# Kernel tuning notes

Measured on AMD Instinct MI355X. Metric: run time of the kernel, lower is better.

The kernel has to match this reference:

```python
import jax, jax.numpy as jnp
import numpy as np

N, F, H, C, HX, E = 50000, 256, 128, 16, 64, 500000
TEMP = 1.0


def gcn_conv(x, src, dst, W, b, n):
    # PyG GCNConv: x @ W, add self-loops, sym-normalized scatter-sum src->dst
    xw = x @ W
    idx = jnp.arange(n)
    s = jnp.concatenate([src, idx])
    d = jnp.concatenate([dst, idx])
    deg = jax.ops.segment_sum(jnp.ones_like(s, dtype=xw.dtype), d, num_segments=n)
    dinv = jnp.where(deg > 0, jax.lax.rsqrt(deg), 0.0)
    norm = dinv[s] * dinv[d]
    out = jax.ops.segment_sum(xw[s] * norm[:, None], d, num_segments=n)
    return out + b


def setup_inputs() -> dict:
    key = jax.random.key(0)
    ks = jax.random.split(key, 16)
    x = jax.random.normal(ks[0], (N, F), jnp.float32)
    edge_index = jax.random.randint(ks[1], (2, E), 0, N)
    neg_edge_index = jax.random.randint(ks[2], (2, E), 0, N)
    y = jax.random.randint(ks[3], (N,), 0, C)
    train_mask = jax.random.uniform(ks[4], (N,)) < 0.5
    def lin(k, fi, fo):
        s = 1.0 / np.sqrt(fi)
        return jax.random.uniform(k, (fi, fo), jnp.float32, -s, s)
    W1 = lin(ks[5], F, H); b1 = jnp.zeros((H,), jnp.float32)
    W2 = lin(ks[6], H, C); b2 = jnp.zeros((C,), jnp.float32)
    Wx = lin(ks[7], F, HX); bx = jnp.zeros((HX,), jnp.float32)
    Wd = lin(ks[8], 2 * (HX + C), 1); bd = jnp.zeros((1,), jnp.float32)
    return dict(x=x, edge_index=edge_index, neg_edge_index=neg_edge_index, y=y,
                train_mask=train_mask, W1=W1, b1=b1, W2=W2, b2=b2,
                Wx=Wx, bx=bx, Wd=Wd, bd=bd)


def reference(x, edge_index, neg_edge_index, y, train_mask,
              W1, b1, W2, b2, Wx, bx, Wd, bd):
    n = x.shape[0]
    # GNN encoder p(y|x,G): 2-layer GCN (eval mode -> dropout identity)
    h = jax.nn.relu(gcn_conv(x, edge_index[0], edge_index[1], W1, b1, n))
    logits = gcn_conv(h, edge_index[0], edge_index[1], W2, b2, n) / TEMP
    y_log_prob = jax.nn.log_softmax(logits, axis=-1)
    y_prob = jnp.where(train_mask[:, None],
                       jax.nn.one_hot(y, logits.shape[-1], dtype=logits.dtype),
                       jnp.exp(y_log_prob))
    # node feature encoder
    xe = jax.nn.relu(x @ Wx + bx)
    def decode(ei):
        s, d = ei[0], ei[1]
        feat = jnp.concatenate([xe[s], xe[d], y_prob[s], y_prob[d]], axis=1)
        return feat @ Wd + bd
    e_pred_pos = decode(edge_index)
    e_pred_neg = decode(neg_edge_index)
    return e_pred_pos, e_pred_neg, y_log_prob
```

## Files before the change

kernel.cpp:

```cpp
#include <hip/hip_runtime.h>

typedef unsigned short ushort_t;
typedef __attribute__((ext_vector_type(8))) short short8;
typedef __attribute__((ext_vector_type(4))) float floatx4;

constexpr int F = 256, H = 128, C = 16, HX = 64;
constexpr int NBCOL = H + HX;

__device__ __forceinline__ ushort_t f2bf(float f) {
  unsigned u = __float_as_uint(f);
  u += 0x7fffu + ((u >> 16) & 1u);
  return (ushort_t)(u >> 16);
}
__device__ __forceinline__ float bflo(unsigned u) { return __uint_as_float(u << 16); }
__device__ __forceinline__ float bfhi(unsigned u) { return __uint_as_float(u & 0xffff0000u); }

__global__ void k_pre(const float* __restrict__ x, ushort_t* __restrict__ xb, int total8,
                      const float* __restrict__ W1, const float* __restrict__ Wx,
                      ushort_t* __restrict__ WBt,
                      const int* __restrict__ dst, int* __restrict__ deg, int e,
                      int nbx, int nbw) {
  int b = blockIdx.x;
  if (b < nbx) {
    int i = b * 256 + threadIdx.x;
    if (i >= total8) return;
    const float4* xp = (const float4*)x;
    float4 a = xp[2 * i], bb = xp[2 * i + 1];
    ushort4 lo = make_ushort4(f2bf(a.x), f2bf(a.y), f2bf(a.z), f2bf(a.w));
    ushort4 hi = make_ushort4(f2bf(bb.x), f2bf(bb.y), f2bf(bb.z), f2bf(bb.w));
    ((ushort4*)xb)[2 * i] = lo;
    ((ushort4*)xb)[2 * i + 1] = hi;
  } else if (b < nbx + nbw) {
    int i = (b - nbx) * 256 + threadIdx.x;
    if (i >= NBCOL * F) return;
    int nn = i / F, k = i % F;
    float v = (nn < H) ? W1[k * H + nn] : Wx[k * HX + (nn - H)];
    WBt[nn * F + k] = f2bf(v);
  } else {
    int i = (b - nbx - nbw) * 256 + threadIdx.x;
    if (i < e) atomicAdd(&deg[dst[i]], 1);
  }
}

__global__ void k_scan_a(const int* __restrict__ deg, int* __restrict__ part, int n) {
  __shared__ int sm[256];
  int i = blockIdx.x * 256 + threadIdx.x;
  int v = (i < n) ? deg[i] : 0;
  sm[threadIdx.x] = v;
  __syncthreads();
  for (int s = 128; s > 0; s >>= 1) {
    if (threadIdx.x < s) sm[threadIdx.x] += sm[threadIdx.x + s];
    __syncthreads();
  }
  if (threadIdx.x == 0) part[blockIdx.x] = sm[0];
}

__global__ void k_scan_b(const int* __restrict__ part, int* __restrict__ blockoff, int nparts) {
  __shared__ int sm[256];
  int t = threadIdx.x;
  int v = (t < nparts) ? part[t] : 0;
  sm[t] = v;
  __syncthreads();
  for (int d = 1; d < 256; d <<= 1) {
    int add = (t >= d) ? sm[t - d] : 0;
    __syncthreads();
    sm[t] += add;
    __syncthreads();
  }
  blockoff[t] = sm[t] - v;
}

__global__ void k_scan_c(const int* __restrict__ deg, const int* __restrict__ blockoff,
                         int* __restrict__ row_start, int* __restrict__ cursor,
                         float* __restrict__ dinv, int n, int e) {
  int i = blockIdx.x * 256 + threadIdx.x;
  int lane = threadIdx.x & 63, wid = threadIdx.x >> 6;
  int v = (i < n) ? deg[i] : 0;
  int x = v;
  for (int d = 1; d < 64; d <<= 1) {
    int t = __shfl_up(x, d);
    if (lane >= d) x += t;
  }
  __shared__ int wsum[4], woff[4];
  if (lane == 63) wsum[wid] = x;
  __syncthreads();
  if (threadIdx.x == 0) {
    int s = 0;
    for (int w = 0; w < 4; w++) { woff[w] = s; s += wsum[w]; }
  }
  __syncthreads();
  int excl = x - v + woff[wid] + blockoff[blockIdx.x];
  if (i < n) {
    row_start[i] = excl;
    cursor[i] = excl;
    dinv[i] = rsqrtf((float)(v + 1));
  }
  if (i == 0) row_start[n] = e;
}

__global__ void k_fill(const int* __restrict__ src, const int* __restrict__ dst,
                       const float* __restrict__ dinv, int* __restrict__ cursor,
                       int2* __restrict__ csr8, int e) {
  int i = blockIdx.x * 256 + threadIdx.x;
  if (i < e) {
    int s = src[i];
    int p = atomicAdd(&cursor[dst[i]], 1);
    csr8[p] = make_int2(s, __float_as_int(dinv[s]));
  }
}

__global__ __launch_bounds__(256, 3) void k_gemm1(const ushort_t* __restrict__ xb,
                                                  const ushort_t* __restrict__ WBt,
                                                  const float* __restrict__ bx,
                                                  ushort_t* __restrict__ xw1,
                                                  float* __restrict__ xe,
                                                  int n, int ntiles) {
  int w = threadIdx.x >> 6, lane = threadIdx.x & 63;
  int q = lane >> 4, l15 = lane & 15;
  const short8* bb = (const short8*)WBt;
  short8 bfr[3][8];
#pragma unroll
  for (int t = 0; t < 3; t++)
#pragma unroll
    for (int kk = 0; kk < 8; kk++)
      bfr[t][kk] = bb[(size_t)(w * 48 + t * 16 + l15) * 32 + kk * 4 + q];

  float bxv[3];
#pragma unroll
  for (int t = 0; t < 3; t++) {
    int g = w * 48 + t * 16;
    bxv[t] = (g >= H) ? bx[g - H + l15] : 0.0f;
  }

  for (int tile = blockIdx.x; tile < ntiles; tile += gridDim.x) {
    int row = tile * 16 + l15;
    const short8* arow = (const short8*)(xb + (size_t)min(row, n - 1) * F);
    short8 a[8];
#pragma unroll
    for (int kk = 0; kk < 8; kk++) a[kk] = arow[kk * 4 + q];

    floatx4 acc0 = (floatx4)(0.0f), acc1 = (floatx4)(0.0f), acc2 = (floatx4)(0.0f);
#pragma unroll
    for (int kk = 0; kk < 8; kk++) {
      acc0 = __builtin_amdgcn_mfma_f32_16x16x32_bf16(a[kk], bfr[0][kk], acc0, 0, 0, 0);
      acc1 = __builtin_amdgcn_mfma_f32_16x16x32_bf16(a[kk], bfr[1][kk], acc1, 0, 0, 0);
      acc2 = __builtin_amdgcn_mfma_f32_16x16x32_bf16(a[kk], bfr[2][kk], acc2, 0, 0, 0);
    }

    floatx4 accs[3] = {acc0, acc1, acc2};
    int rbase = tile * 16 + q * 4;
#pragma unroll
    for (int t = 0; t < 3; t++) {
      int g = w * 48 + t * 16;
#pragma unroll
      for (int r = 0; r < 4; r++) {
        int ro = rbase + r;
        if (ro < n) {
          if (g < H) {
            xw1[(size_t)ro * H + g + l15] = f2bf(accs[t][r]);
          } else {
            xe[(size_t)ro * HX + (g - H) + l15] = fmaxf(accs[t][r] + bxv[t], 0.0f);
          }
        }
      }
    }
  }
}

__global__ void k_agg1(const ushort_t* __restrict__ xw1, const int* __restrict__ row_start,
                       const int2* __restrict__ csr8, const float* __restrict__ dinv,
                       const float* __restrict__ b1, ushort_t* __restrict__ hb, int n) {
  int v = blockIdx.x * 4 + (threadIdx.x >> 6);
  if (v >= n) return;
  int lane = threadIdx.x & 63;
  float dv = dinv[v];
  unsigned sv = ((const unsigned*)(xw1 + (size_t)v * H))[lane];
  float ax = dv * bflo(sv), ay = dv * bfhi(sv);
  int j0 = row_start[v], j1 = row_start[v + 1];
  int j = j0;
  for (; j + 8 <= j1; j += 8) {
    int2 ee[8];
    unsigned rr[8];
#pragma unroll
    for (int u = 0; u < 8; u++) ee[u] = csr8[j + u];
#pragma unroll
    for (int u = 0; u < 8; u++)
      rr[u] = ((const unsigned*)(xw1 + (size_t)ee[u].x * H))[lane];
#pragma unroll
    for (int u = 0; u < 8; u++) {
      float wu = __int_as_float(ee[u].y);
      ax += wu * bflo(rr[u]);
      ay += wu * bfhi(rr[u]);
    }
  }
  for (; j < j1; j++) {
    int2 e0 = csr8[j];
    unsigned r0 = ((const unsigned*)(xw1 + (size_t)e0.x * H))[lane];
    float w0 = __int_as_float(e0.y);
    ax += w0 * bflo(r0);
    ay += w0 * bfhi(r0);
  }
  int c = lane * 2;
  float o0 = fmaxf(dv * ax + b1[c], 0.0f);
  float o1 = fmaxf(dv * ay + b1[c + 1], 0.0f);
  unsigned hv = (unsigned)f2bf(o0) | ((unsigned)f2bf(o1) << 16);
  ((unsigned*)(hb + (size_t)v * H))[lane] = hv;
}

__global__ void k_gemm2(const ushort_t* __restrict__ hb, const float* __restrict__ W2,
                        float* __restrict__ hw2, int n) {
  int idx = blockIdx.x * 256 + threadIdx.x;
  int node = idx >> 2, cg = idx & 3;
  if (node >= n) return;
  float a0 = 0, a1 = 0, a2 = 0, a3 = 0;
  const unsigned* hr = (const unsigned*)(hb + (size_t)node * H);
#pragma unroll 8
  for (int k2 = 0; k2 < 64; k2++) {
    unsigned u = hr[k2];
    float h0 = bflo(u), h1 = bfhi(u);
    float4 w0 = *(const float4*)(W2 + (2 * k2) * C + cg * 4);
    float4 w1 = *(const float4*)(W2 + (2 * k2 + 1) * C + cg * 4);
    a0 += h0 * w0.x + h1 * w1.x;
    a1 += h0 * w0.y + h1 * w1.y;
    a2 += h0 * w0.z + h1 * w1.z;
    a3 += h0 * w0.w + h1 * w1.w;
  }
  *(float4*)(hw2 + (size_t)node * C + cg * 4) = make_float4(a0, a1, a2, a3);
}

__global__ void k_agg2ab(const float* __restrict__ hw2, const int* __restrict__ row_start,
                         const int2* __restrict__ csr8, const float* __restrict__ dinv,
                         const float* __restrict__ b2, const int* __restrict__ y,
                         const int* __restrict__ tmask, const float* __restrict__ xe,
                         const float* __restrict__ Wd, float* __restrict__ ylp_out,
                         float* __restrict__ Aarr, float* __restrict__ Barr, int n) {
  int idx = blockIdx.x * 256 + threadIdx.x;
  int node = idx >> 4, c = idx & 15;
  if (node >= n) return;
  float dv = dinv[node];
  float acc = dv * hw2[(size_t)node * C + c];
  int j0 = row_start[node], j1 = row_start[node + 1];
  int j = j0;
  for (; j + 8 <= j1; j += 8) {
    int2 ee[8];
    float rr[8];
#pragma unroll
    for (int u = 0; u < 8; u++) ee[u] = csr8[j + u];
#pragma unroll
    for (int u = 0; u < 8; u++) rr[u] = hw2[(size_t)ee[u].x * C + c];
#pragma unroll
    for (int u = 0; u < 8; u++) acc += __int_as_float(ee[u].y) * rr[u];
  }
  for (; j + 4 <= j1; j += 4) {
    int2 e0 = csr8[j], e1 = csr8[j + 1], e2 = csr8[j + 2], e3 = csr8[j + 3];
    float r0 = hw2[(size_t)e0.x * C + c];
    float r1 = hw2[(size_t)e1.x * C + c];
    float r2 = hw2[(size_t)e2.x * C + c];
    float r3 = hw2[(size_t)e3.x * C + c];
    acc += __int_as_float(e0.y) * r0 + __int_as_float(e1.y) * r1 +
           __int_as_float(e2.y) * r2 + __int_as_float(e3.y) * r3;
  }
  for (; j < j1; j++) {
    int2 e0 = csr8[j];
    acc += __int_as_float(e0.y) * hw2[(size_t)e0.x * C + c];
  }
  float logit = dv * acc + b2[c];
  float m = logit;
  for (int o = 8; o > 0; o >>= 1) m = fmaxf(m, __shfl_xor(m, o, 16));
  float e = expf(logit - m);
  float s16 = e;
  for (int o = 8; o > 0; o >>= 1) s16 += __shfl_xor(s16, o, 16);
  float lp = (logit - m) - logf(s16);
  ylp_out[(size_t)node * C + c] = lp;
  float yp = tmask[node] ? ((y[node] == c) ? 1.0f : 0.0f) : (e / s16);

  float4 xv = *(const float4*)(xe + (size_t)node * HX + c * 4);
  float4 wa = *(const float4*)(Wd + c * 4);
  float4 wb = *(const float4*)(Wd + HX + c * 4);
  float pa = xv.x * wa.x + xv.y * wa.y + xv.z * wa.z + xv.w * wa.w + yp * Wd[2 * HX + c];
  float pb = xv.x * wb.x + xv.y * wb.y + xv.z * wb.z + xv.w * wb.w + yp * Wd[2 * HX + C + c];
  for (int o = 8; o > 0; o >>= 1) {
    pa += __shfl_xor(pa, o, 16);
    pb += __shfl_xor(pb, o, 16);
  }
  if (c == 0) { Aarr[node] = pa; Barr[node] = pb; }
}

__global__ void k_decode(const int* __restrict__ ei, const int* __restrict__ nei,
                         const float* __restrict__ Aarr, const float* __restrict__ Barr,
                         const float* __restrict__ bd, float* __restrict__ out, int e) {
  int i = blockIdx.x * 256 + threadIdx.x;
  if (i >= 2 * e) return;
  float b0 = bd[0];
  if (i < e) {
    int s = ei[i], d = ei[e + i];
    out[i] = Aarr[s] + Barr[d] + b0;
  } else {
    int j = i - e;
    int s = nei[j], d = nei[e + j];
    out[e + j] = Aarr[s] + Barr[d] + b0;
  }
}

extern "C" void kernel_launch(void* const* d_in, const int* in_sizes, int n_in,
                              void* d_out, int out_size, void* d_ws, size_t ws_size,
                              hipStream_t stream) {
  const float* x = (const float*)d_in[0];
  const int* ei = (const int*)d_in[1];
  const int* nei = (const int*)d_in[2];
  const int* y = (const int*)d_in[3];
  const int* tmask = (const int*)d_in[4];
  const float* W1 = (const float*)d_in[5];
  const float* b1 = (const float*)d_in[6];
  const float* W2 = (const float*)d_in[7];
  const float* b2 = (const float*)d_in[8];
  const float* Wx = (const float*)d_in[9];
  const float* bx = (const float*)d_in[10];
  const float* Wd = (const float*)d_in[11];
  const float* bd = (const float*)d_in[12];
  float* out = (float*)d_out;

  int n = in_sizes[3];
  int e = in_sizes[1] / 2;

  char* ws = (char*)d_ws;
  size_t off = 0;
  auto alloc = [&](size_t bytes) -> void* {
    void* p = ws + off;
    off += (bytes + 511) & ~(size_t)511;
    return p;
  };
  ushort_t* xb = (ushort_t*)alloc((size_t)n * F * 2);
  ushort_t* WBt = (ushort_t*)alloc((size_t)NBCOL * F * 2);
  ushort_t* xw1 = (ushort_t*)alloc((size_t)n * H * 2);
  float* xe = (float*)alloc((size_t)n * HX * 4);
  ushort_t* hb = (ushort_t*)alloc((size_t)n * H * 2);
  float* hw2 = (float*)alloc((size_t)n * C * 4);
  float* dinv = (float*)alloc((size_t)n * 4);
  int* deg = (int*)alloc((size_t)n * 4);
  int* row_start = (int*)alloc((size_t)(n + 1) * 4);
  int* cursor = (int*)alloc((size_t)n * 4);
  int2* csr8 = (int2*)alloc((size_t)e * 8);
  int* part = (int*)alloc(1024 * 4);
  int* blockoff = (int*)alloc(1024 * 4);
  float* Aarr = (float*)alloc((size_t)n * 4);
  float* Barr = (float*)alloc((size_t)n * 4);

  const int* src = ei;
  const int* dst = ei + e;

  hipMemsetAsync(deg, 0, (size_t)n * 4, stream);

  int total8 = n * F / 8;
  int nbx = (total8 + 255) / 256;
  int nbw = (NBCOL * F + 255) / 256;
  int nbe = (e + 255) / 256;
  k_pre<<<nbx + nbw + nbe, 256, 0, stream>>>(x, xb, total8, W1, Wx, WBt, dst, deg, e,
                                             nbx, nbw);

  int nblk = (n + 255) / 256;
  k_scan_a<<<nblk, 256, 0, stream>>>(deg, part, n);
  k_scan_b<<<1, 256, 0, stream>>>(part, blockoff, nblk);
  k_scan_c<<<nblk, 256, 0, stream>>>(deg, blockoff, row_start, cursor, dinv, n, e);
  k_fill<<<(e + 255) / 256, 256, 0, stream>>>(src, dst, dinv, cursor, csr8, e);

  int ntiles = (n + 15) / 16;
  int ggrid = ntiles < 768 ? ntiles : 768;
  k_gemm1<<<ggrid, 256, 0, stream>>>(xb, WBt, bx, xw1, xe, n, ntiles);
  k_agg1<<<(n + 3) / 4, 256, 0, stream>>>(xw1, row_start, csr8, dinv, b1, hb, n);
  k_gemm2<<<(n * 4 + 255) / 256, 256, 0, stream>>>(hb, W2, hw2, n);
  k_agg2ab<<<(n * 16 + 255) / 256, 256, 0, stream>>>(hw2, row_start, csr8, dinv, b2, y,
                                                     tmask, xe, Wd, out + (size_t)2 * e,
                                                     Aarr, Barr, n);
  k_decode<<<(2 * e + 255) / 256, 256, 0, stream>>>(ei, nei, Aarr, Barr, bd, out, e);
}
```

Baseline: 269.8 us.

## Fuse preprocessing, CSR build and GEMM1 into persistent kernel; fuse agg1 with GEMM2

Merges the conversion, degree counting, three scan kernels, CSR fill and the first GEMM into one persistent 512-block kernel. The stages are separated by atomic-counter grid barriers. The first aggregation now does the H×C projection through shared memory, so the bf16 hidden buffer and the separate GEMM2 launch are gone. The goal is to cut launch overhead and one intermediate global round trip. In exchange it relies on all 512 blocks being co-resident for the spin barriers, and the GEMM phase runs at fewer blocks and lower occupancy than before.

```diff
diff --git a/kernel.cpp b/kernel.cpp
--- a/kernel.cpp
+++ b/kernel.cpp
@@ -15,107 +15,111 @@
 __device__ __forceinline__ float bflo(unsigned u) { return __uint_as_float(u << 16); }
 __device__ __forceinline__ float bfhi(unsigned u) { return __uint_as_float(u & 0xffff0000u); }
 
-__global__ void k_pre(const float* __restrict__ x, ushort_t* __restrict__ xb, int total8,
-                      const float* __restrict__ W1, const float* __restrict__ Wx,
-                      ushort_t* __restrict__ WBt,
-                      const int* __restrict__ dst, int* __restrict__ deg, int e,
-                      int nbx, int nbw) {
-  int b = blockIdx.x;
-  if (b < nbx) {
-    int i = b * 256 + threadIdx.x;
-    if (i >= total8) return;
-    const float4* xp = (const float4*)x;
+__device__ __forceinline__ void gbar(int* cnt) {
+  __threadfence();
+  __syncthreads();
+  if (threadIdx.x == 0) {
+    __hip_atomic_fetch_add(cnt, 1, __ATOMIC_ACQ_REL, __HIP_MEMORY_SCOPE_AGENT);
+    while (__hip_atomic_load(cnt, __ATOMIC_ACQUIRE, __HIP_MEMORY_SCOPE_AGENT) <
+           (int)gridDim.x)
+      __builtin_amdgcn_s_sleep(2);
+  }
+  __syncthreads();
+}
+
+__global__ __launch_bounds__(256, 2) void k_build(
+    const float* __restrict__ x, ushort_t* __restrict__ xb, int total8,
+    const float* __restrict__ W1, const float* __restrict__ Wx,
+    ushort_t* __restrict__ WBt, const int* __restrict__ src,
+    const int* __restrict__ dst, int* __restrict__ deg, int e,
+    int* __restrict__ part, int* __restrict__ blockoff,
+    int* __restrict__ row_start, int* __restrict__ cursor,
+    float* __restrict__ dinv, int2* __restrict__ csr8,
+    const float* __restrict__ bx, ushort_t* __restrict__ xw1,
+    float* __restrict__ xe, int* __restrict__ bar, int n, int ntiles) {
+  __shared__ int sm[256];
+  __shared__ int wsum[4], woff[4];
+  int tid = blockIdx.x * 256 + threadIdx.x;
+  int nthreads = gridDim.x * 256;
+  int lane = threadIdx.x & 63, wid = threadIdx.x >> 6;
+
+  const float4* xp = (const float4*)x;
+  for (int i = tid; i < total8; i += nthreads) {
     float4 a = xp[2 * i], bb = xp[2 * i + 1];
     ushort4 lo = make_ushort4(f2bf(a.x), f2bf(a.y), f2bf(a.z), f2bf(a.w));
     ushort4 hi = make_ushort4(f2bf(bb.x), f2bf(bb.y), f2bf(bb.z), f2bf(bb.w));
     ((ushort4*)xb)[2 * i] = lo;
     ((ushort4*)xb)[2 * i + 1] = hi;
-  } else if (b < nbx + nbw) {
-    int i = (b - nbx) * 256 + threadIdx.x;
-    if (i >= NBCOL * F) return;
+  }
+  for (int i = tid; i < NBCOL * F; i += nthreads) {
     int nn = i / F, k = i % F;
     float v = (nn < H) ? W1[k * H + nn] : Wx[k * HX + (nn - H)];
     WBt[nn * F + k] = f2bf(v);
-  } else {
-    int i = (b - nbx - nbw) * 256 + threadIdx.x;
-    if (i < e) atomicAdd(&deg[dst[i]], 1);
-  }
-}
-
-__global__ void k_scan_a(const int* __restrict__ deg, int* __restrict__ part, int n) {
-  __shared__ int sm[256];
-  int i = blockIdx.x * 256 + threadIdx.x;
-  int v = (i < n) ? deg[i] : 0;
-  sm[threadIdx.x] = v;
-  __syncthreads();
-  for (int s = 128; s > 0; s >>= 1) {
-    if (threadIdx.x < s) sm[threadIdx.x] += sm[threadIdx.x + s];
-    __syncthreads();
-  }
-  if (threadIdx.x == 0) part[blockIdx.x] = sm[0];
-}
-
-__global__ void k_scan_b(const int* __restrict__ part, int* __restrict__ blockoff, int nparts) {
-  __shared__ int sm[256];
-  int t = threadIdx.x;
-  int v = (t < nparts) ? part[t] : 0;
-  sm[t] = v;
-  __syncthreads();
-  for (int d = 1; d < 256; d <<= 1) {
-    int add = (t >= d) ? sm[t - d] : 0;
-    __syncthreads();
-    sm[t] += add;
-    __syncthreads();
-  }
-  blockoff[t] = sm[t] - v;
-}
-
-__global__ void k_scan_c(const int* __restrict__ deg, const int* __restrict__ blockoff,
-                         int* __restrict__ row_start, int* __restrict__ cursor,
-                         float* __restrict__ dinv, int n, int e) {
-  int i = blockIdx.x * 256 + threadIdx.x;
-  int lane = threadIdx.x & 63, wid = threadIdx.x >> 6;
-  int v = (i < n) ? deg[i] : 0;
-  int x = v;
-  for (int d = 1; d < 64; d <<= 1) {
-    int t = __shfl_up(x, d);
-    if (lane >= d) x += t;
-  }
-  __shared__ int wsum[4], woff[4];
-  if (lane == 63) wsum[wid] = x;
-  __syncthreads();
-  if (threadIdx.x == 0) {
-    int s = 0;
-    for (int w = 0; w < 4; w++) { woff[w] = s; s += wsum[w]; }
-  }
-  __syncthreads();
-  int excl = x - v + woff[wid] + blockoff[blockIdx.x];
-  if (i < n) {
-    row_start[i] = excl;
-    cursor[i] = excl;
-    dinv[i] = rsqrtf((float)(v + 1));
-  }
-  if (i == 0) row_start[n] = e;
-}
-
-__global__ void k_fill(const int* __restrict__ src, const int* __restrict__ dst,
-                       const float* __restrict__ dinv, int* __restrict__ cursor,
-                       int2* __restrict__ csr8, int e) {
-  int i = blockIdx.x * 256 + threadIdx.x;
-  if (i < e) {
+  }
+  for (int i = tid; i < e; i += nthreads) atomicAdd(&deg[dst[i]], 1);
+  gbar(&bar[0]);
+
+  int nchunk = (n + 255) / 256;
+  for (int c = blockIdx.x; c < nchunk; c += gridDim.x) {
+    int i = c * 256 + threadIdx.x;
+    sm[threadIdx.x] = (i < n) ? deg[i] : 0;
+    __syncthreads();
+    for (int s = 128; s > 0; s >>= 1) {
+      if (threadIdx.x < s) sm[threadIdx.x] += sm[threadIdx.x + s];
+      __syncthreads();
+    }
+    if (threadIdx.x == 0) part[c] = sm[0];
+    __syncthreads();
+  }
+  gbar(&bar[1]);
+
+  if (blockIdx.x == 0) {
+    int t = threadIdx.x;
+    int v = (t < nchunk) ? part[t] : 0;
+    sm[t] = v;
+    __syncthreads();
+    for (int d = 1; d < 256; d <<= 1) {
+      int add = (t >= d) ? sm[t - d] : 0;
+      __syncthreads();
+      sm[t] += add;
+      __syncthreads();
+    }
+    blockoff[t] = sm[t] - v;
+  }
+  gbar(&bar[2]);
+
+  for (int c = blockIdx.x; c < nchunk; c += gridDim.x) {
+    int i = c * 256 + threadIdx.x;
+    int v = (i < n) ? deg[i] : 0;
+    int xs = v;
+    for (int d = 1; d < 64; d <<= 1) {
+      int t = __shfl_up(xs, d);
+      if (lane >= d) xs += t;
+    }
+    if (lane == 63) wsum[wid] = xs;
+    __syncthreads();
+    if (threadIdx.x == 0) {
+      int s = 0;
+      for (int w = 0; w < 4; w++) { woff[w] = s; s += wsum[w]; }
+    }
+    __syncthreads();
+    int excl = xs - v + woff[wid] + blockoff[c];
+    if (i < n) {
+      row_start[i] = excl;
+      cursor[i] = excl;
+      dinv[i] = rsqrtf((float)(v + 1));
+    }
+    __syncthreads();
+  }
+  if (tid == 0) row_start[n] = e;
+  gbar(&bar[3]);
+
+  for (int i = tid; i < e; i += nthreads) {
     int s = src[i];
     int p = atomicAdd(&cursor[dst[i]], 1);
     csr8[p] = make_int2(s, __float_as_int(dinv[s]));
   }
-}
-
-__global__ __launch_bounds__(256, 3) void k_gemm1(const ushort_t* __restrict__ xb,
-                                                  const ushort_t* __restrict__ WBt,
-                                                  const float* __restrict__ bx,
-                                                  ushort_t* __restrict__ xw1,
-                                                  float* __restrict__ xe,
-                                                  int n, int ntiles) {
-  int w = threadIdx.x >> 6, lane = threadIdx.x & 63;
+
   int q = lane >> 4, l15 = lane & 15;
   const short8* bb = (const short8*)WBt;
   short8 bfr[3][8];
@@ -123,22 +127,19 @@
   for (int t = 0; t < 3; t++)
 #pragma unroll
     for (int kk = 0; kk < 8; kk++)
-      bfr[t][kk] = bb[(size_t)(w * 48 + t * 16 + l15) * 32 + kk * 4 + q];
-
+      bfr[t][kk] = bb[(size_t)(wid * 48 + t * 16 + l15) * 32 + kk * 4 + q];
   float bxv[3];
 #pragma unroll
   for (int t = 0; t < 3; t++) {
-    int g = w * 48 + t * 16;
+    int g = wid * 48 + t * 16;
     bxv[t] = (g >= H) ? bx[g - H + l15] : 0.0f;
   }
-
   for (int tile = blockIdx.x; tile < ntiles; tile += gridDim.x) {
     int row = tile * 16 + l15;
     const short8* arow = (const short8*)(xb + (size_t)min(row, n - 1) * F);
     short8 a[8];
 #pragma unroll
     for (int kk = 0; kk < 8; kk++) a[kk] = arow[kk * 4 + q];
-
     floatx4 acc0 = (floatx4)(0.0f), acc1 = (floatx4)(0.0f), acc2 = (floatx4)(0.0f);
 #pragma unroll
     for (int kk = 0; kk < 8; kk++) {
@@ -146,12 +147,11 @@
       acc1 = __builtin_amdgcn_mfma_f32_16x16x32_bf16(a[kk], bfr[1][kk], acc1, 0, 0, 0);
       acc2 = __builtin_amdgcn_mfma_f32_16x16x32_bf16(a[kk], bfr[2][kk], acc2, 0, 0, 0);
     }
-
     floatx4 accs[3] = {acc0, acc1, acc2};
     int rbase = tile * 16 + q * 4;
 #pragma unroll
     for (int t = 0; t < 3; t++) {
-      int g = w * 48 + t * 16;
+      int g = wid * 48 + t * 16;
 #pragma unroll
       for (int r = 0; r < 4; r++) {
         int ro = rbase + r;
@@ -167,10 +167,13 @@
   }
 }
 
-__global__ void k_agg1(const ushort_t* __restrict__ xw1, const int* __restrict__ row_start,
-                       const int2* __restrict__ csr8, const float* __restrict__ dinv,
-                       const float* __restrict__ b1, ushort_t* __restrict__ hb, int n) {
-  int v = blockIdx.x * 4 + (threadIdx.x >> 6);
+__global__ void k_agg1g2(const ushort_t* __restrict__ xw1, const int* __restrict__ row_start,
+                         const int2* __restrict__ csr8, const float* __restrict__ dinv,
+                         const float* __restrict__ b1, const float* __restrict__ W2,
+                         float* __restrict__ hw2, int n) {
+  __shared__ float2 hsm[4][64];
+  int wid = threadIdx.x >> 6;
+  int v = blockIdx.x * 4 + wid;
   if (v >= n) return;
   int lane = threadIdx.x & 63;
   float dv = dinv[v];
@@ -200,32 +203,20 @@
     ax += w0 * bflo(r0);
     ay += w0 * bfhi(r0);
   }
-  int c = lane * 2;
-  float o0 = fmaxf(dv * ax + b1[c], 0.0f);
-  float o1 = fmaxf(dv * ay + b1[c + 1], 0.0f);
-  unsigned hv = (unsigned)f2bf(o0) | ((unsigned)f2bf(o1) << 16);
-  ((unsigned*)(hb + (size_t)v * H))[lane] = hv;
-}
-
-__global__ void k_gemm2(const ushort_t* __restrict__ hb, const float* __restrict__ W2,
-                        float* __restrict__ hw2, int n) {
-  int idx = blockIdx.x * 256 + threadIdx.x;
-  int node = idx >> 2, cg = idx & 3;
-  if (node >= n) return;
-  float a0 = 0, a1 = 0, a2 = 0, a3 = 0;
-  const unsigned* hr = (const unsigned*)(hb + (size_t)node * H);
-#pragma unroll 8
-  for (int k2 = 0; k2 < 64; k2++) {
-    unsigned u = hr[k2];
-    float h0 = bflo(u), h1 = bfhi(u);
-    float4 w0 = *(const float4*)(W2 + (2 * k2) * C + cg * 4);
-    float4 w1 = *(const float4*)(W2 + (2 * k2 + 1) * C + cg * 4);
-    a0 += h0 * w0.x + h1 * w1.x;
-    a1 += h0 * w0.y + h1 * w1.y;
-    a2 += h0 * w0.z + h1 * w1.z;
-    a3 += h0 * w0.w + h1 * w1.w;
-  }
-  *(float4*)(hw2 + (size_t)node * C + cg * 4) = make_float4(a0, a1, a2, a3);
+  int c2 = lane * 2;
+  float o0 = fmaxf(dv * ax + b1[c2], 0.0f);
+  float o1 = fmaxf(dv * ay + b1[c2 + 1], 0.0f);
+  hsm[wid][lane] = make_float2(o0, o1);
+
+  int c = lane & 15, g = lane >> 4;
+  const float* hrow = (const float*)hsm[wid];
+  float p = 0.0f;
+#pragma unroll
+  for (int jj = 0; jj < 32; jj++)
+    p += hrow[g * 32 + jj] * W2[(g * 32 + jj) * C + c];
+  p += __shfl_xor(p, 16);
+  p += __shfl_xor(p, 32);
+  if (g == 0) hw2[(size_t)v * C + c] = p;
 }
 
 __global__ void k_agg2ab(const float* __restrict__ hw2, const int* __restrict__ row_start,
@@ -330,14 +321,14 @@
     off += (bytes + 511) & ~(size_t)511;
     return p;
   };
+  int* bar = (int*)alloc(512);
+  int* deg = (int*)alloc((size_t)n * 4);
   ushort_t* xb = (ushort_t*)alloc((size_t)n * F * 2);
   ushort_t* WBt = (ushort_t*)alloc((size_t)NBCOL * F * 2);
   ushort_t* xw1 = (ushort_t*)alloc((size_t)n * H * 2);
   float* xe = (float*)alloc((size_t)n * HX * 4);
-  ushort_t* hb = (ushort_t*)alloc((size_t)n * H * 2);
   float* hw2 = (float*)alloc((size_t)n * C * 4);
   float* dinv = (float*)alloc((size_t)n * 4);
-  int* deg = (int*)alloc((size_t)n * 4);
   int* row_start = (int*)alloc((size_t)(n + 1) * 4);
   int* cursor = (int*)alloc((size_t)n * 4);
   int2* csr8 = (int2*)alloc((size_t)e * 8);
@@ -349,26 +340,14 @@
   const int* src = ei;
   const int* dst = ei + e;
 
-  hipMemsetAsync(deg, 0, (size_t)n * 4, stream);
+  hipMemsetAsync(bar, 0, 512 + (size_t)n * 4, stream);
 
   int total8 = n * F / 8;
-  int nbx = (total8 + 255) / 256;
-  int nbw = (NBCOL * F + 255) / 256;
-  int nbe = (e + 255) / 256;
-  k_pre<<<nbx + nbw + nbe, 256, 0, stream>>>(x, xb, total8, W1, Wx, WBt, dst, deg, e,
-                                             nbx, nbw);
-
-  int nblk = (n + 255) / 256;
-  k_scan_a<<<nblk, 256, 0, stream>>>(deg, part, n);
-  k_scan_b<<<1, 256, 0, stream>>>(part, blockoff, nblk);
-  k_scan_c<<<nblk, 256, 0, stream>>>(deg, blockoff, row_start, cursor, dinv, n, e);
-  k_fill<<<(e + 255) / 256, 256, 0, stream>>>(src, dst, dinv, cursor, csr8, e);
-
   int ntiles = (n + 15) / 16;
-  int ggrid = ntiles < 768 ? ntiles : 768;
-  k_gemm1<<<ggrid, 256, 0, stream>>>(xb, WBt, bx, xw1, xe, n, ntiles);
-  k_agg1<<<(n + 3) / 4, 256, 0, stream>>>(xw1, row_start, csr8, dinv, b1, hb, n);
-  k_gemm2<<<(n * 4 + 255) / 256, 256, 0, stream>>>(hb, W2, hw2, n);
+  k_build<<<512, 256, 0, stream>>>(x, xb, total8, W1, Wx, WBt, src, dst, deg, e,
+                                   part, blockoff, row_start, cursor, dinv, csr8,
+                                   bx, xw1, xe, bar, n, ntiles);
+  k_agg1g2<<<(n + 3) / 4, 256, 0, stream>>>(xw1, row_start, csr8, dinv, b1, W2, hw2, n);
   k_agg2ab<<<(n * 16 + 255) / 256, 256, 0, stream>>>(hw2, row_start, csr8, dinv, b2, y,
                                                      tmask, xe, Wd, out + (size_t)2 * e,
                                                      Aarr, Barr, n);
```

Result: slower. 472.6 us (+75.2%).
